# Kernel tuning notes

Hardware: AMD Instinct MI355X
Metric: run time of the kernel (lower is better)

## Reference

```python
import jax, jax.numpy as jnp
import numpy as np

B, N, D, H = 8, 1024, 512, 8
HEAD_DIM = D // H


def setup_inputs() -> dict:
    key = jax.random.key(0)
    k1, k2, k3, k4 = jax.random.split(key, 4)
    x = jax.random.normal(k1, (B, N, D), dtype=jnp.float32)
    relative_bias_logits = jax.random.normal(k2, (B, N, N, H), dtype=jnp.float32)
    # Dense params (fan-in scaled like lecun init)
    W_qkv = jax.random.normal(k3, (D, 3 * D), dtype=jnp.float32) / np.sqrt(D)
    b_qkv = jnp.zeros((3 * D,), dtype=jnp.float32)
    W_o = jax.random.normal(k4, (D, D), dtype=jnp.float32) / np.sqrt(D)
    b_o = jnp.zeros((D,), dtype=jnp.float32)
    return {"x": x, "relative_bias_logits": relative_bias_logits,
            "W_qkv": W_qkv, "b_qkv": b_qkv, "W_o": W_o, "b_o": b_o}


def reference(x, relative_bias_logits, W_qkv, b_qkv, W_o, b_o):
    # x: (B, N, D); relative_bias_logits: (B, N, N, H)
    n_heads = relative_bias_logits.shape[-1]
    emb = x.shape[-1]
    head_dim = emb // n_heads
    n = x.shape[-2]
    batch_dim = x.shape[:-2]

    qkv = x @ W_qkv + b_qkv                                   # (B, N, 3D)
    qkv = qkv.reshape(*batch_dim, n, n_heads, 3, head_dim)    # (B, N, H, 3, T)
    q, k, v = qkv[..., 0, :], qkv[..., 1, :], qkv[..., 2, :]  # each (B, N, H, T)

    logits = jnp.einsum('...QHT,...KHT->...QKH', q, k) / jnp.sqrt(
        jnp.asarray(head_dim, dtype=x.dtype))
    logits = logits + relative_bias_logits                    # (B, Q, K, H)
    # softmax over the K axis (axis=-2); jax.nn.softmax is max-stable
    attention = jax.nn.softmax(logits, axis=-2)
    # dropout deterministic (train=False): identity
    y = jnp.einsum('...QKH,...KHT->...QHT', attention, v)     # (B, N, H, T)
    y = y.reshape(*batch_dim, n, emb)                          # (B, N, D)
    y = y @ W_o + b_o
    return y
```

## Files before the change

kernel.cpp:

```cpp
#include <hip/hip_runtime.h>

typedef unsigned short u16;
typedef __attribute__((ext_vector_type(8))) short short8;
typedef __attribute__((ext_vector_type(4))) float f32x4;

__device__ __forceinline__ u16 f2bf(float f) {
  union { float f; unsigned u; } c; c.f = f;
  unsigned u = c.u;
  return (u16)((u + 0x7FFFu + ((u >> 16) & 1u)) >> 16);
}

__global__ __launch_bounds__(256) void cvt_x_kernel(const float* __restrict__ x,
                                                    u16* __restrict__ xb) {
  int i = blockIdx.x * 256 + threadIdx.x;
  float4 v = ((const float4*)x)[i];
  uint2 st;
  st.x = (unsigned)f2bf(v.x) | ((unsigned)f2bf(v.y) << 16);
  st.y = (unsigned)f2bf(v.z) | ((unsigned)f2bf(v.w) << 16);
  ((uint2*)xb)[i] = st;
}

__global__ __launch_bounds__(256) void transp_kernel(const float* __restrict__ W,
                                                     u16* __restrict__ Wt,
                                                     int NC, int total) {
  int idx = blockIdx.x * 256 + threadIdx.x;
  if (idx >= total) return;
  int n = idx >> 9, k = idx & 511;
  Wt[idx] = f2bf(W[(size_t)k * NC + n]);
}

template<int MODE>
__global__ __launch_bounds__(256) void gemm_kernel(
    const u16* __restrict__ A, const u16* __restrict__ Bt,
    const float* __restrict__ biasv,
    u16* __restrict__ qb, u16* __restrict__ kb, u16* __restrict__ vtb,
    float* __restrict__ outp) {
  __shared__ u16 As[64 * 64];
  __shared__ u16 Bs[64 * 64];
  const int tid = threadIdx.x;
  const int lane = tid & 63;
  const int w = tid >> 6, wm = w >> 1, wn = w & 1;
  const int m0 = blockIdx.y * 64, n0 = blockIdx.x * 64;
  const int r = tid >> 3, s = tid & 7;
  const int lm = lane & 15, lg = lane >> 4;
  f32x4 acc[2][2] = {};

  for (int k0 = 0; k0 < 512; k0 += 64) {
    __syncthreads();
    *(uint4*)&As[r * 64 + s * 8]        = *(const uint4*)&A[(size_t)(m0 + r) * 512 + k0 + s * 8];
    *(uint4*)&As[(r + 32) * 64 + s * 8] = *(const uint4*)&A[(size_t)(m0 + r + 32) * 512 + k0 + s * 8];
    *(uint4*)&Bs[r * 64 + s * 8]        = *(const uint4*)&Bt[(size_t)(n0 + r) * 512 + k0 + s * 8];
    *(uint4*)&Bs[(r + 32) * 64 + s * 8] = *(const uint4*)&Bt[(size_t)(n0 + r + 32) * 512 + k0 + s * 8];
    __syncthreads();
#pragma unroll
    for (int tc = 0; tc < 2; tc++) {
      short8 bfr[2];
#pragma unroll
      for (int nt = 0; nt < 2; nt++)
        bfr[nt] = *(const short8*)&Bs[(wn * 32 + nt * 16 + lm) * 64 + tc * 32 + lg * 8];
#pragma unroll
      for (int mt = 0; mt < 2; mt++) {
        short8 af = *(const short8*)&As[(wm * 32 + mt * 16 + lm) * 64 + tc * 32 + lg * 8];
#pragma unroll
        for (int nt = 0; nt < 2; nt++)
          acc[mt][nt] = __builtin_amdgcn_mfma_f32_16x16x32_bf16(af, bfr[nt], acc[mt][nt], 0, 0, 0);
      }
    }
  }

#pragma unroll
  for (int mt = 0; mt < 2; mt++) {
#pragma unroll
    for (int nt = 0; nt < 2; nt++) {
      const int col = n0 + wn * 32 + nt * 16 + lm;
      const float bv = biasv[col];
#pragma unroll
      for (int r2 = 0; r2 < 4; r2++) {
        const int row = m0 + wm * 32 + mt * 16 + lg * 4 + r2;
        const float v = acc[mt][nt][r2] + bv;
        if (MODE == 0) {
          const int h = col / 192, rem = col % 192;
          const int which = rem >> 6, t = rem & 63;
          const int b = row >> 10, n = row & 1023;
          const u16 bb = f2bf(v);
          if (which == 0)      qb[((size_t)(b * 8 + h) * 1024 + n) * 64 + t] = bb;
          else if (which == 1) kb[((size_t)(b * 8 + h) * 1024 + n) * 64 + t] = bb;
          else                 vtb[((size_t)(b * 8 + h) * 64 + t) * 1024 + n] = bb;
        } else {
          outp[(size_t)row * 512 + col] = v;
        }
      }
    }
  }
}

__global__ __launch_bounds__(512) void attn_kernel(
    const u16* __restrict__ qb, const u16* __restrict__ kb,
    const u16* __restrict__ vtb, const float* __restrict__ bias,
    u16* __restrict__ yb) {
  __shared__ float biasS[8 * 32 * 34];
  __shared__ u16 Ps[8 * 32 * 40];
  const int tid = threadIdx.x;
  const int lane = tid & 63;
  const int h = tid >> 6;
  const int b = blockIdx.y;
  const int q0 = blockIdx.x * 32;
  const size_t bh = (size_t)b * 8 + h;
  const u16* Q  = qb  + bh * (1024 * 64);
  const u16* K  = kb  + bh * (1024 * 64);
  const u16* VT = vtb + bh * (64 * 1024);
  const int lm = lane & 15, lg = lane >> 4;

  short8 aq[2][2];
#pragma unroll
  for (int mt = 0; mt < 2; mt++)
#pragma unroll
    for (int tc = 0; tc < 2; tc++)
      aq[mt][tc] = *(const short8*)&Q[(size_t)(q0 + mt * 16 + lm) * 64 + tc * 32 + lg * 8];

  f32x4 o[2][4] = {};
  float mrow[2][4], lrow[2][4];
#pragma unroll
  for (int mt = 0; mt < 2; mt++)
#pragma unroll
    for (int r2 = 0; r2 < 4; r2++) { mrow[mt][r2] = -1e30f; lrow[mt][r2] = 0.f; }

  const float SC   = 0.125f * 1.4426950408889634f;
  const float LG2E = 1.4426950408889634f;

  const int kl = lane >> 1, h4 = (lane & 1) * 4;
  float4 pre[4];
#pragma unroll
  for (int rr = 0; rr < 4; rr++) {
    const int qr = h + rr * 8;
    pre[rr] = *(const float4*)&bias[(((size_t)(b * 1024 + q0 + qr)) * 1024 + kl) * 8 + h4];
  }

  for (int kc = 0; kc < 1024; kc += 32) {
    __syncthreads();
#pragma unroll
    for (int rr = 0; rr < 4; rr++) {
      const int qr = h + rr * 8;
      biasS[(h4 + 0) * 1088 + qr * 34 + kl] = pre[rr].x;
      biasS[(h4 + 1) * 1088 + qr * 34 + kl] = pre[rr].y;
      biasS[(h4 + 2) * 1088 + qr * 34 + kl] = pre[rr].z;
      biasS[(h4 + 3) * 1088 + qr * 34 + kl] = pre[rr].w;
    }
    __syncthreads();
    if (kc + 32 < 1024) {
#pragma unroll
      for (int rr = 0; rr < 4; rr++) {
        const int qr = h + rr * 8;
        pre[rr] = *(const float4*)&bias[(((size_t)(b * 1024 + q0 + qr)) * 1024 + (kc + 32) + kl) * 8 + h4];
      }
    }

    f32x4 sf[2][2];
#pragma unroll
    for (int kt = 0; kt < 2; kt++) {
      short8 bk[2];
#pragma unroll
      for (int tc = 0; tc < 2; tc++)
        bk[tc] = *(const short8*)&K[(size_t)(kc + kt * 16 + lm) * 64 + tc * 32 + lg * 8];
#pragma unroll
      for (int mt = 0; mt < 2; mt++) {
        f32x4 c = {0.f, 0.f, 0.f, 0.f};
        c = __builtin_amdgcn_mfma_f32_16x16x32_bf16(aq[mt][0], bk[0], c, 0, 0, 0);
        c = __builtin_amdgcn_mfma_f32_16x16x32_bf16(aq[mt][1], bk[1], c, 0, 0, 0);
        sf[mt][kt] = c;
      }
    }

#pragma unroll
    for (int mt = 0; mt < 2; mt++) {
      float pv2[2][4];
      const int qrb = mt * 16 + lg * 4;
#pragma unroll
      for (int kt = 0; kt < 2; kt++)
#pragma unroll
        for (int r2 = 0; r2 < 4; r2++)
          pv2[kt][r2] = sf[mt][kt][r2] * SC +
                        biasS[h * 1088 + (qrb + r2) * 34 + kt * 16 + lm] * LG2E;
      float rmax[4];
#pragma unroll
      for (int r2 = 0; r2 < 4; r2++) rmax[r2] = fmaxf(pv2[0][r2], pv2[1][r2]);
#pragma unroll
      for (int d = 1; d < 16; d <<= 1)
#pragma unroll
        for (int r2 = 0; r2 < 4; r2++)
          rmax[r2] = fmaxf(rmax[r2], __shfl_xor(rmax[r2], d));
      float alpha[4];
#pragma unroll
      for (int r2 = 0; r2 < 4; r2++) {
        const float mn = fmaxf(mrow[mt][r2], rmax[r2]);
        alpha[r2] = exp2f(mrow[mt][r2] - mn);
        mrow[mt][r2] = mn;
      }
      float rsum[4] = {0.f, 0.f, 0.f, 0.f};
#pragma unroll
      for (int kt = 0; kt < 2; kt++)
#pragma unroll
        for (int r2 = 0; r2 < 4; r2++) {
          const float p = exp2f(pv2[kt][r2] - mrow[mt][r2]);
          pv2[kt][r2] = p;
          rsum[r2] += p;
        }
#pragma unroll
      for (int d = 1; d < 16; d <<= 1)
#pragma unroll
        for (int r2 = 0; r2 < 4; r2++)
          rsum[r2] += __shfl_xor(rsum[r2], d);
#pragma unroll
      for (int r2 = 0; r2 < 4; r2++)
        lrow[mt][r2] = lrow[mt][r2] * alpha[r2] + rsum[r2];
#pragma unroll
      for (int nt = 0; nt < 4; nt++)
#pragma unroll
        for (int r2 = 0; r2 < 4; r2++)
          o[mt][nt][r2] *= alpha[r2];
#pragma unroll
      for (int kt = 0; kt < 2; kt++)
#pragma unroll
        for (int r2 = 0; r2 < 4; r2++)
          Ps[h * 1280 + (qrb + r2) * 40 + kt * 16 + lm] = f2bf(pv2[kt][r2]);
    }

    short8 bv[4];
#pragma unroll
    for (int nt = 0; nt < 4; nt++)
      bv[nt] = *(const short8*)&VT[(size_t)(nt * 16 + lm) * 1024 + kc + lg * 8];
#pragma unroll
    for (int mt = 0; mt < 2; mt++) {
      short8 ap = *(const short8*)&Ps[h * 1280 + (mt * 16 + lm) * 40 + lg * 8];
#pragma unroll
      for (int nt = 0; nt < 4; nt++)
        o[mt][nt] = __builtin_amdgcn_mfma_f32_16x16x32_bf16(ap, bv[nt], o[mt][nt], 0, 0, 0);
    }
  }

#pragma unroll
  for (int mt = 0; mt < 2; mt++)
#pragma unroll
    for (int nt = 0; nt < 4; nt++)
#pragma unroll
      for (int r2 = 0; r2 < 4; r2++) {
        const int row = q0 + mt * 16 + lg * 4 + r2;
        const float yv = o[mt][nt][r2] / lrow[mt][r2];
        yb[((size_t)(b * 1024 + row)) * 512 + h * 64 + nt * 16 + lm] = f2bf(yv);
      }
}

extern "C" void kernel_launch(void* const* d_in, const int* in_sizes, int n_in,
                              void* d_out, int out_size, void* d_ws, size_t ws_size,
                              hipStream_t stream) {
  const float* x    = (const float*)d_in[0];
  const float* bias = (const float*)d_in[1];
  const float* Wqkv = (const float*)d_in[2];
  const float* bqkv = (const float*)d_in[3];
  const float* Wo   = (const float*)d_in[4];
  const float* bo   = (const float*)d_in[5];
  float* out = (float*)d_out;

  char* p = (char*)d_ws;
  u16* xb    = (u16*)p; p += (size_t)8192 * 512 * 2;
  u16* wqkvT = (u16*)p; p += (size_t)1536 * 512 * 2;
  u16* woT   = (u16*)p; p += (size_t)512 * 512 * 2;
  u16* qB    = (u16*)p; p += (size_t)8 * 8 * 1024 * 64 * 2;
  u16* kB    = (u16*)p; p += (size_t)8 * 8 * 1024 * 64 * 2;
  u16* vtB   = (u16*)p; p += (size_t)8 * 8 * 64 * 1024 * 2;
  u16* yB    = (u16*)p; p += (size_t)8192 * 512 * 2;

  cvt_x_kernel<<<4096, 256, 0, stream>>>(x, xb);
  transp_kernel<<<3072, 256, 0, stream>>>(Wqkv, wqkvT, 1536, 1536 * 512);
  transp_kernel<<<1024, 256, 0, stream>>>(Wo, woT, 512, 512 * 512);
  gemm_kernel<0><<<dim3(24, 128), 256, 0, stream>>>(xb, wqkvT, bqkv, qB, kB, vtB, nullptr);
  attn_kernel<<<dim3(32, 8), 512, 0, stream>>>(qB, kB, vtB, bias, yB);
  gemm_kernel<1><<<dim3(8, 128), 256, 0, stream>>>(yB, woT, bo, nullptr, nullptr, nullptr, out);
}
```

Measured before the change: 512.8 us.

## Halve attention query tile, enlarge GEMM tiles with direct-to-LDS loads, tile weight transpose

The attention kernel now processes 16 query rows per block instead of 32, doubling the grid to expose more parallelism for the bandwidth-bound bias stream. The projection GEMMs switch to 128x128 tiles with 4x4 MFMA accumulators per wave and load via global_load_lds. The weight transpose uses a shared-memory tile for coalesced reads and writes. Smaller attention tiles re-read K/V more often, and larger GEMM tiles reduce block count and may lower occupancy.

```diff
diff --git a/kernel.cpp b/kernel.cpp
--- a/kernel.cpp
+++ b/kernel.cpp
@@ -8,6 +8,12 @@
   union { float f; unsigned u; } c; c.f = f;
   unsigned u = c.u;
   return (u16)((u + 0x7FFFu + ((u >> 16) & 1u)) >> 16);
+}
+
+__device__ __forceinline__ void gload_lds16(const void* g, void* l) {
+  __builtin_amdgcn_global_load_lds(
+      (const __attribute__((address_space(1))) unsigned int*)g,
+      (__attribute__((address_space(3))) unsigned int*)l, 16, 0, 0);
 }
 
 __global__ __launch_bounds__(256) void cvt_x_kernel(const float* __restrict__ x,
@@ -21,12 +27,17 @@
 }
 
 __global__ __launch_bounds__(256) void transp_kernel(const float* __restrict__ W,
-                                                     u16* __restrict__ Wt,
-                                                     int NC, int total) {
-  int idx = blockIdx.x * 256 + threadIdx.x;
-  if (idx >= total) return;
-  int n = idx >> 9, k = idx & 511;
-  Wt[idx] = f2bf(W[(size_t)k * NC + n]);
+                                                     u16* __restrict__ Wt, int NC) {
+  __shared__ float T[32][33];
+  const int n0 = blockIdx.x * 32, k0 = blockIdx.y * 32;
+  const int tx = threadIdx.x & 31, ty = threadIdx.x >> 5;
+#pragma unroll
+  for (int i = 0; i < 4; i++)
+    T[ty + 8 * i][tx] = W[(size_t)(k0 + ty + 8 * i) * NC + n0 + tx];
+  __syncthreads();
+#pragma unroll
+  for (int i = 0; i < 4; i++)
+    Wt[(size_t)(n0 + ty + 8 * i) * 512 + k0 + tx] = f2bf(T[tx][ty + 8 * i]);
 }
 
 template<int MODE>
@@ -35,48 +46,50 @@
     const float* __restrict__ biasv,
     u16* __restrict__ qb, u16* __restrict__ kb, u16* __restrict__ vtb,
     float* __restrict__ outp) {
-  __shared__ u16 As[64 * 64];
-  __shared__ u16 Bs[64 * 64];
+  __shared__ u16 As[128 * 64];
+  __shared__ u16 Bs[128 * 64];
   const int tid = threadIdx.x;
   const int lane = tid & 63;
   const int w = tid >> 6, wm = w >> 1, wn = w & 1;
-  const int m0 = blockIdx.y * 64, n0 = blockIdx.x * 64;
-  const int r = tid >> 3, s = tid & 7;
+  const int m0 = blockIdx.y * 128, n0 = blockIdx.x * 128;
+  const int lr = lane >> 3, ls = lane & 7;
   const int lm = lane & 15, lg = lane >> 4;
-  f32x4 acc[2][2] = {};
+  f32x4 acc[4][4] = {};
 
   for (int k0 = 0; k0 < 512; k0 += 64) {
     __syncthreads();
-    *(uint4*)&As[r * 64 + s * 8]        = *(const uint4*)&A[(size_t)(m0 + r) * 512 + k0 + s * 8];
-    *(uint4*)&As[(r + 32) * 64 + s * 8] = *(const uint4*)&A[(size_t)(m0 + r + 32) * 512 + k0 + s * 8];
-    *(uint4*)&Bs[r * 64 + s * 8]        = *(const uint4*)&Bt[(size_t)(n0 + r) * 512 + k0 + s * 8];
-    *(uint4*)&Bs[(r + 32) * 64 + s * 8] = *(const uint4*)&Bt[(size_t)(n0 + r + 32) * 512 + k0 + s * 8];
+#pragma unroll
+    for (int j = 0; j < 4; j++) {
+      const int rowb = w * 32 + j * 8;
+      gload_lds16(&A[(size_t)(m0 + rowb + lr) * 512 + k0 + ls * 8], &As[rowb * 64]);
+      gload_lds16(&Bt[(size_t)(n0 + rowb + lr) * 512 + k0 + ls * 8], &Bs[rowb * 64]);
+    }
     __syncthreads();
 #pragma unroll
     for (int tc = 0; tc < 2; tc++) {
-      short8 bfr[2];
-#pragma unroll
-      for (int nt = 0; nt < 2; nt++)
-        bfr[nt] = *(const short8*)&Bs[(wn * 32 + nt * 16 + lm) * 64 + tc * 32 + lg * 8];
-#pragma unroll
-      for (int mt = 0; mt < 2; mt++) {
-        short8 af = *(const short8*)&As[(wm * 32 + mt * 16 + lm) * 64 + tc * 32 + lg * 8];
-#pragma unroll
-        for (int nt = 0; nt < 2; nt++)
-          acc[mt][nt] = __builtin_amdgcn_mfma_f32_16x16x32_bf16(af, bfr[nt], acc[mt][nt], 0, 0, 0);
+      short8 af[4], bf[4];
+#pragma unroll
+      for (int t = 0; t < 4; t++) {
+        af[t] = *(const short8*)&As[(wm * 64 + t * 16 + lm) * 64 + tc * 32 + lg * 8];
+        bf[t] = *(const short8*)&Bs[(wn * 64 + t * 16 + lm) * 64 + tc * 32 + lg * 8];
       }
-    }
-  }
-
-#pragma unroll
-  for (int mt = 0; mt < 2; mt++) {
-#pragma unroll
-    for (int nt = 0; nt < 2; nt++) {
-      const int col = n0 + wn * 32 + nt * 16 + lm;
+#pragma unroll
+      for (int mt = 0; mt < 4; mt++)
+#pragma unroll
+        for (int nt = 0; nt < 4; nt++)
+          acc[mt][nt] = __builtin_amdgcn_mfma_f32_16x16x32_bf16(af[mt], bf[nt], acc[mt][nt], 0, 0, 0);
+    }
+  }
+
+#pragma unroll
+  for (int mt = 0; mt < 4; mt++) {
+#pragma unroll
+    for (int nt = 0; nt < 4; nt++) {
+      const int col = n0 + wn * 64 + nt * 16 + lm;
       const float bv = biasv[col];
 #pragma unroll
       for (int r2 = 0; r2 < 4; r2++) {
-        const int row = m0 + wm * 32 + mt * 16 + lg * 4 + r2;
+        const int row = m0 + wm * 64 + mt * 16 + lg * 4 + r2;
         const float v = acc[mt][nt][r2] + bv;
         if (MODE == 0) {
           const int h = col / 192, rem = col % 192;
@@ -98,156 +111,142 @@
     const u16* __restrict__ qb, const u16* __restrict__ kb,
     const u16* __restrict__ vtb, const float* __restrict__ bias,
     u16* __restrict__ yb) {
-  __shared__ float biasS[8 * 32 * 34];
-  __shared__ u16 Ps[8 * 32 * 40];
+  __shared__ float biasS[8 * 544];
+  __shared__ u16 Ps[8 * 16 * 40];
   const int tid = threadIdx.x;
   const int lane = tid & 63;
   const int h = tid >> 6;
   const int b = blockIdx.y;
-  const int q0 = blockIdx.x * 32;
+  const int q0 = blockIdx.x * 16;
   const size_t bh = (size_t)b * 8 + h;
   const u16* Q  = qb  + bh * (1024 * 64);
   const u16* K  = kb  + bh * (1024 * 64);
   const u16* VT = vtb + bh * (64 * 1024);
   const int lm = lane & 15, lg = lane >> 4;
 
-  short8 aq[2][2];
-#pragma unroll
-  for (int mt = 0; mt < 2; mt++)
-#pragma unroll
-    for (int tc = 0; tc < 2; tc++)
-      aq[mt][tc] = *(const short8*)&Q[(size_t)(q0 + mt * 16 + lm) * 64 + tc * 32 + lg * 8];
-
-  f32x4 o[2][4] = {};
-  float mrow[2][4], lrow[2][4];
-#pragma unroll
-  for (int mt = 0; mt < 2; mt++)
-#pragma unroll
-    for (int r2 = 0; r2 < 4; r2++) { mrow[mt][r2] = -1e30f; lrow[mt][r2] = 0.f; }
+  short8 aq[2];
+#pragma unroll
+  for (int tc = 0; tc < 2; tc++)
+    aq[tc] = *(const short8*)&Q[(size_t)(q0 + lm) * 64 + tc * 32 + lg * 8];
+
+  f32x4 o[4] = {};
+  float mrow[4], lrow[4];
+#pragma unroll
+  for (int r2 = 0; r2 < 4; r2++) { mrow[r2] = -1e30f; lrow[r2] = 0.f; }
 
   const float SC   = 0.125f * 1.4426950408889634f;
   const float LG2E = 1.4426950408889634f;
 
-  const int kl = lane >> 1, h4 = (lane & 1) * 4;
-  float4 pre[4];
-#pragma unroll
-  for (int rr = 0; rr < 4; rr++) {
-    const int qr = h + rr * 8;
-    pre[rr] = *(const float4*)&bias[(((size_t)(b * 1024 + q0 + qr)) * 1024 + kl) * 8 + h4];
-  }
+  const float4* b4 = (const float4*)bias;
+  int qi[2], kk[2], hf[2];
+#pragma unroll
+  for (int p = 0; p < 2; p++) {
+    const int idx = p * 512 + tid;
+    qi[p] = idx >> 6; kk[p] = (idx & 63) >> 1; hf[p] = idx & 1;
+  }
+  float4 pre[2];
+#pragma unroll
+  for (int p = 0; p < 2; p++)
+    pre[p] = b4[((size_t)(b * 1024 + q0 + qi[p]) * 1024 + kk[p]) * 2 + hf[p]];
 
   for (int kc = 0; kc < 1024; kc += 32) {
     __syncthreads();
 #pragma unroll
-    for (int rr = 0; rr < 4; rr++) {
-      const int qr = h + rr * 8;
-      biasS[(h4 + 0) * 1088 + qr * 34 + kl] = pre[rr].x;
-      biasS[(h4 + 1) * 1088 + qr * 34 + kl] = pre[rr].y;
-      biasS[(h4 + 2) * 1088 + qr * 34 + kl] = pre[rr].z;
-      biasS[(h4 + 3) * 1088 + qr * 34 + kl] = pre[rr].w;
+    for (int p = 0; p < 2; p++) {
+      const float* pf = (const float*)&pre[p];
+      const int base = qi[p] * 34 + kk[p];
+#pragma unroll
+      for (int j = 0; j < 4; j++)
+        biasS[(hf[p] * 4 + j) * 544 + base] = pf[j];
     }
     __syncthreads();
     if (kc + 32 < 1024) {
 #pragma unroll
-      for (int rr = 0; rr < 4; rr++) {
-        const int qr = h + rr * 8;
-        pre[rr] = *(const float4*)&bias[(((size_t)(b * 1024 + q0 + qr)) * 1024 + (kc + 32) + kl) * 8 + h4];
-      }
-    }
-
-    f32x4 sf[2][2];
+      for (int p = 0; p < 2; p++)
+        pre[p] = b4[((size_t)(b * 1024 + q0 + qi[p]) * 1024 + (kc + 32) + kk[p]) * 2 + hf[p]];
+    }
+
+    f32x4 s2[2];
 #pragma unroll
     for (int kt = 0; kt < 2; kt++) {
       short8 bk[2];
 #pragma unroll
       for (int tc = 0; tc < 2; tc++)
         bk[tc] = *(const short8*)&K[(size_t)(kc + kt * 16 + lm) * 64 + tc * 32 + lg * 8];
-#pragma unroll
-      for (int mt = 0; mt < 2; mt++) {
-        f32x4 c = {0.f, 0.f, 0.f, 0.f};
-        c = __builtin_amdgcn_mfma_f32_16x16x32_bf16(aq[mt][0], bk[0], c, 0, 0, 0);
-        c = __builtin_amdgcn_mfma_f32_16x16x32_bf16(aq[mt][1], bk[1], c, 0, 0, 0);
-        sf[mt][kt] = c;
+      f32x4 c = {0.f, 0.f, 0.f, 0.f};
+      c = __builtin_amdgcn_mfma_f32_16x16x32_bf16(aq[0], bk[0], c, 0, 0, 0);
+      c = __builtin_amdgcn_mfma_f32_16x16x32_bf16(aq[1], bk[1], c, 0, 0, 0);
+      s2[kt] = c;
+    }
+
+    float pv2[2][4];
+#pragma unroll
+    for (int kt = 0; kt < 2; kt++)
+#pragma unroll
+      for (int r2 = 0; r2 < 4; r2++)
+        pv2[kt][r2] = s2[kt][r2] * SC +
+                      biasS[h * 544 + (lg * 4 + r2) * 34 + kt * 16 + lm] * LG2E;
+    float rmax[4];
+#pragma unroll
+    for (int r2 = 0; r2 < 4; r2++) rmax[r2] = fmaxf(pv2[0][r2], pv2[1][r2]);
+#pragma unroll
+    for (int d = 1; d < 16; d <<= 1)
+#pragma unroll
+      for (int r2 = 0; r2 < 4; r2++)
+        rmax[r2] = fmaxf(rmax[r2], __shfl_xor(rmax[r2], d));
+    float alpha[4];
+#pragma unroll
+    for (int r2 = 0; r2 < 4; r2++) {
+      const float mn = fmaxf(mrow[r2], rmax[r2]);
+      alpha[r2] = exp2f(mrow[r2] - mn);
+      mrow[r2] = mn;
+    }
+    float rsum[4] = {0.f, 0.f, 0.f, 0.f};
+#pragma unroll
+    for (int kt = 0; kt < 2; kt++)
+#pragma unroll
+      for (int r2 = 0; r2 < 4; r2++) {
+        const float p = exp2f(pv2[kt][r2] - mrow[r2]);
+        pv2[kt][r2] = p;
+        rsum[r2] += p;
       }
-    }
-
-#pragma unroll
-    for (int mt = 0; mt < 2; mt++) {
-      float pv2[2][4];
-      const int qrb = mt * 16 + lg * 4;
-#pragma unroll
-      for (int kt = 0; kt < 2; kt++)
-#pragma unroll
-        for (int r2 = 0; r2 < 4; r2++)
-          pv2[kt][r2] = sf[mt][kt][r2] * SC +
-                        biasS[h * 1088 + (qrb + r2) * 34 + kt * 16 + lm] * LG2E;
-      float rmax[4];
-#pragma unroll
-      for (int r2 = 0; r2 < 4; r2++) rmax[r2] = fmaxf(pv2[0][r2], pv2[1][r2]);
-#pragma unroll
-      for (int d = 1; d < 16; d <<= 1)
-#pragma unroll
-        for (int r2 = 0; r2 < 4; r2++)
-          rmax[r2] = fmaxf(rmax[r2], __shfl_xor(rmax[r2], d));
-      float alpha[4];
-#pragma unroll
-      for (int r2 = 0; r2 < 4; r2++) {
-        const float mn = fmaxf(mrow[mt][r2], rmax[r2]);
-        alpha[r2] = exp2f(mrow[mt][r2] - mn);
-        mrow[mt][r2] = mn;
-      }
-      float rsum[4] = {0.f, 0.f, 0.f, 0.f};
-#pragma unroll
-      for (int kt = 0; kt < 2; kt++)
-#pragma unroll
-        for (int r2 = 0; r2 < 4; r2++) {
-          const float p = exp2f(pv2[kt][r2] - mrow[mt][r2]);
-          pv2[kt][r2] = p;
-          rsum[r2] += p;
-        }
-#pragma unroll
-      for (int d = 1; d < 16; d <<= 1)
-#pragma unroll
-        for (int r2 = 0; r2 < 4; r2++)
-          rsum[r2] += __shfl_xor(rsum[r2], d);
-#pragma unroll
-      for (int r2 = 0; r2 < 4; r2++)
-        lrow[mt][r2] = lrow[mt][r2] * alpha[r2] + rsum[r2];
-#pragma unroll
-      for (int nt = 0; nt < 4; nt++)
-#pragma unroll
-        for (int r2 = 0; r2 < 4; r2++)
-          o[mt][nt][r2] *= alpha[r2];
-#pragma unroll
-      for (int kt = 0; kt < 2; kt++)
-#pragma unroll
-        for (int r2 = 0; r2 < 4; r2++)
-          Ps[h * 1280 + (qrb + r2) * 40 + kt * 16 + lm] = f2bf(pv2[kt][r2]);
-    }
+#pragma unroll
+    for (int d = 1; d < 16; d <<= 1)
+#pragma unroll
+      for (int r2 = 0; r2 < 4; r2++)
+        rsum[r2] += __shfl_xor(rsum[r2], d);
+#pragma unroll
+    for (int r2 = 0; r2 < 4; r2++)
+      lrow[r2] = lrow[r2] * alpha[r2] + rsum[r2];
+#pragma unroll
+    for (int nt = 0; nt < 4; nt++)
+#pragma unroll
+      for (int r2 = 0; r2 < 4; r2++)
+        o[nt][r2] *= alpha[r2];
+#pragma unroll
+    for (int kt = 0; kt < 2; kt++)
+#pragma unroll
+      for (int r2 = 0; r2 < 4; r2++)
+        Ps[h * 640 + (lg * 4 + r2) * 40 + kt * 16 + lm] = f2bf(pv2[kt][r2]);
 
     short8 bv[4];
 #pragma unroll
     for (int nt = 0; nt < 4; nt++)
       bv[nt] = *(const short8*)&VT[(size_t)(nt * 16 + lm) * 1024 + kc + lg * 8];
-#pragma unroll
-    for (int mt = 0; mt < 2; mt++) {
-      short8 ap = *(const short8*)&Ps[h * 1280 + (mt * 16 + lm) * 40 + lg * 8];
-#pragma unroll
-      for (int nt = 0; nt < 4; nt++)
-        o[mt][nt] = __builtin_amdgcn_mfma_f32_16x16x32_bf16(ap, bv[nt], o[mt][nt], 0, 0, 0);
-    }
-  }
-
-#pragma unroll
-  for (int mt = 0; mt < 2; mt++)
+    short8 ap = *(const short8*)&Ps[h * 640 + lm * 40 + lg * 8];
 #pragma unroll
     for (int nt = 0; nt < 4; nt++)
-#pragma unroll
-      for (int r2 = 0; r2 < 4; r2++) {
-        const int row = q0 + mt * 16 + lg * 4 + r2;
-        const float yv = o[mt][nt][r2] / lrow[mt][r2];
-        yb[((size_t)(b * 1024 + row)) * 512 + h * 64 + nt * 16 + lm] = f2bf(yv);
-      }
+      o[nt] = __builtin_amdgcn_mfma_f32_16x16x32_bf16(ap, bv[nt], o[nt], 0, 0, 0);
+  }
+
+#pragma unroll
+  for (int nt = 0; nt < 4; nt++)
+#pragma unroll
+    for (int r2 = 0; r2 < 4; r2++) {
+      const int row = q0 + lg * 4 + r2;
+      const float yv = o[nt][r2] / lrow[r2];
+      yb[((size_t)(b * 1024 + row)) * 512 + h * 64 + nt * 16 + lm] = f2bf(yv);
+    }
 }
 
 extern "C" void kernel_launch(void* const* d_in, const int* in_sizes, int n_in,
@@ -271,9 +270,9 @@
   u16* yB    = (u16*)p; p += (size_t)8192 * 512 * 2;
 
   cvt_x_kernel<<<4096, 256, 0, stream>>>(x, xb);
-  transp_kernel<<<3072, 256, 0, stream>>>(Wqkv, wqkvT, 1536, 1536 * 512);
-  transp_kernel<<<1024, 256, 0, stream>>>(Wo, woT, 512, 512 * 512);
-  gemm_kernel<0><<<dim3(24, 128), 256, 0, stream>>>(xb, wqkvT, bqkv, qB, kB, vtB, nullptr);
-  attn_kernel<<<dim3(32, 8), 512, 0, stream>>>(qB, kB, vtB, bias, yB);
-  gemm_kernel<1><<<dim3(8, 128), 256, 0, stream>>>(yB, woT, bo, nullptr, nullptr, nullptr, out);
-}
+  transp_kernel<<<dim3(48, 16), 256, 0, stream>>>(Wqkv, wqkvT, 1536);
+  transp_kernel<<<dim3(16, 16), 256, 0, stream>>>(Wo, woT, 512);
+  gemm_kernel<0><<<dim3(12, 64), 256, 0, stream>>>(xb, wqkvT, bqkv, qB, kB, vtB, nullptr);
+  attn_kernel<<<dim3(64, 8), 512, 0, stream>>>(qB, kB, vtB, bias, yB);
+  gemm_kernel<1><<<dim3(4, 64), 256, 0, stream>>>(yB, woT, bo, nullptr, nullptr, nullptr, out);
+}
```

New measurement: 518.8 us. No clear change (+1.2%).
